# Performance work log

Hardware: AMD Instinct MI355X
Metric: run time of the kernel (lower is better)

## Reference

```python
import jax, jax.numpy as jnp
import numpy as np

B, CIN, T = 32, 16, 4096
H, DEPTH, E, K = 192, 4, 4, 7
DILATIONS = (1, 2, 4, 8)
NUM_BANDS, P = 16, 8
HM = 2 * H  # mlp_ratio = 2.0
NCLS = 50
GAIN_LIMIT = 0.5
EPS = 1e-5


def _rbf_basis(num_bins, num_bands):
    freqs = jnp.linspace(0.0, 1.0, num_bins)
    centers = jnp.linspace(0.0, 1.0, num_bands)
    width = 1.5 / (num_bands - 1)
    basis = jnp.exp(-0.5 * ((freqs[None, :] - centers[:, None]) / width) ** 2)
    return basis / jnp.clip(basis.sum(-1, keepdims=True), 1e-8)


def _layernorm(x, g, b):
    m = x.mean(-1, keepdims=True)
    v = x.var(-1, keepdims=True)
    return (x - m) / jnp.sqrt(v + EPS) * g + b


def _groupnorm1(x, g, b):
    # GroupNorm(1, C): normalize over (C, T) per sample, per-channel affine
    m = x.mean((1, 2), keepdims=True)
    v = x.var((1, 2), keepdims=True)
    return (x - m) / jnp.sqrt(v + EPS) * g[None, :, None] + b[None, :, None]


def _bn_eval(x, g, b):
    # eval-mode BatchNorm1d with running_mean=0, running_var=1
    return x * (g / jnp.sqrt(1.0 + EPS))[None, :, None] + b[None, :, None]


def _gelu(x):
    return jax.nn.gelu(x, approximate=False)


def _dwconv(x, w, dilation):
    pad = (K // 2) * dilation
    return jax.lax.conv_general_dilated(
        x, w, (1,), [(pad, pad)], rhs_dilation=(dilation,),
        dimension_numbers=("NCH", "OIH", "NCH"), feature_group_count=x.shape[1])


def setup_inputs() -> dict:
    key = jax.random.key(0)
    ks = jax.random.split(key, 12)
    return {
        "x": jax.random.normal(ks[0], (B, CIN, T), jnp.float32),
        "stem_w": jax.random.normal(ks[1], (H, CIN, 3)) * 0.1,
        "stem_bn_g": jnp.ones((H,)), "stem_bn_b": jnp.zeros((H,)),
        "ln_g": jnp.ones((NUM_BANDS,)), "ln_b": jnp.zeros((NUM_BANDS,)),
        "proj_w": jax.random.normal(ks[2], (NUM_BANDS, NUM_BANDS)) * 0.25,
        "prototypes": jax.random.normal(ks[3], (P, NUM_BANDS)) * 0.02,
        "route_lib": jax.random.normal(ks[4], (P, DEPTH, E)) * 0.1,
        "gain_lib": jax.random.normal(ks[5], (P, DEPTH, H)) * 0.1,
        "norm1_g": jnp.ones((DEPTH, H)), "norm1_b": jnp.zeros((DEPTH, H)),
        "expert_w": jax.random.normal(ks[6], (DEPTH, E, H, 1, K)) * 0.2,
        "mix_w": jax.random.normal(ks[7], (DEPTH, H, H)) * (1.0 / np.sqrt(H)),
        "mix_bn_g": jnp.ones((DEPTH, H)), "mix_bn_b": jnp.zeros((DEPTH, H)),
        "norm2_g": jnp.ones((DEPTH, H)), "norm2_b": jnp.zeros((DEPTH, H)),
        "mlp_w1": jax.random.normal(ks[8], (DEPTH, HM, H)) * (1.0 / np.sqrt(H)),
        "mlp_b1": jnp.zeros((DEPTH, HM)),
        "mlp_w2": jax.random.normal(ks[9], (DEPTH, H, HM)) * (1.0 / np.sqrt(HM)),
        "mlp_b2": jnp.zeros((DEPTH, H)),
        "head_w": jax.random.normal(ks[10], (NCLS, H)) * (1.0 / np.sqrt(H)),
        "head_b": jnp.zeros((NCLS,)),
    }


def reference(x, stem_w, stem_bn_g, stem_bn_b, ln_g, ln_b, proj_w, prototypes,
              route_lib, gain_lib, norm1_g, norm1_b, expert_w, mix_w, mix_bn_g,
              mix_bn_b, norm2_g, norm2_b, mlp_w1, mlp_b1, mlp_w2, mlp_b2,
              head_w, head_b):
    # --- SpectralSummary ---
    spec = jnp.fft.rfft(x.astype(jnp.float32), axis=-1, norm="ortho")
    mag = jnp.abs(spec).mean(axis=1)                      # [B, bins]
    basis = _rbf_basis(mag.shape[-1], NUM_BANDS)          # [bands, bins]
    summary = jnp.log1p(mag) @ basis.T                    # [B, bands]
    # --- PrototypeRouter ---
    s = _layernorm(summary, ln_g, ln_b)
    rs = s @ proj_w.T
    logits = -((rs[:, None, :] - prototypes[None]) ** 2).mean(-1)  # [B, P]
    assign = jax.nn.softmax(logits * np.sqrt(NUM_BANDS), axis=-1)
    routes = jax.nn.softmax(jnp.einsum("bp,pde->bde", assign, route_lib), axis=-1)  # [B,D,E]
    gains = 1.0 + GAIN_LIMIT * jnp.tanh(jnp.einsum("bp,pdc->bdc", assign, gain_lib))  # [B,D,C]
    # --- Backbone stem ---
    z = jax.lax.conv_general_dilated(x, stem_w, (1,), [(1, 1)],
                                     dimension_numbers=("NCH", "OIH", "NCH"))
    z = _gelu(_bn_eval(z, stem_bn_g, stem_bn_b))
    # --- Routed temporal blocks ---
    for d in range(DEPTH):
        zn = _groupnorm1(z, norm1_g[d], norm1_b[d])
        pieces = jnp.stack([_dwconv(zn, expert_w[d, e], DILATIONS[e]) for e in range(E)], axis=1)  # [B,E,C,T]
        mixed = jnp.einsum("be,bect->bct", routes[:, d], pieces)
        mixed = mixed * gains[:, d][:, :, None]
        mixed = _gelu(_bn_eval(jnp.einsum("oc,bct->bot", mix_w[d], mixed), mix_bn_g[d], mix_bn_b[d]))
        z = z + mixed
        zn2 = _groupnorm1(z, norm2_g[d], norm2_b[d])
        h = _gelu(jnp.einsum("oc,bct->bot", mlp_w1[d], zn2) + mlp_b1[d][None, :, None])
        z = z + jnp.einsum("oc,bct->bot", mlp_w2[d], h) + mlp_b2[d][None, :, None]
    # --- Head: global average pool + linear ---
    pooled = z.mean(-1)
    return pooled @ head_w.T + head_b
```

## Files before the change

### kernel.cpp

```cpp
#include <hip/hip_runtime.h>
#include <math.h>

constexpr int cB = 32, cCIN = 16, cT = 4096, cH = 192, cD = 4, cE = 4, cK = 7;
constexpr int cBANDS = 16, cP = 8, cHM = 384, cNCLS = 50, cBINS = 2049;
constexpr float cEPS = 1e-5f;
constexpr int TT = 64, HALO = 24;
constexpr int ZSTR = 112;
constexpr int NTAP = 19;
constexpr float INV_SQRT2 = 0.7071067811865475f;

typedef __bf16 bf16_t;
typedef bf16_t bf16x8 __attribute__((ext_vector_type(8)));
typedef float f32x4 __attribute__((ext_vector_type(4)));

constexpr int OFFS[NTAP] = {-24,-16,-12,-8,-6,-4,-3,-2,-1,0,1,2,3,4,6,8,12,16,24};
constexpr int IDXT[cE][cK] = {
    {6, 7, 8, 9, 10, 11, 12},
    {4, 5, 7, 9, 11, 13, 14},
    {2, 3, 5, 9, 13, 15, 16},
    {0, 1, 3, 9, 15, 17, 18}};

__device__ __forceinline__ int xcd_swz(int bid) {
    return (bid & 7) * 256 + (bid >> 3);
}

__device__ __forceinline__ float fast_erf(float x) {
    float ax = fabsf(x);
    float t = 1.0f / fmaf(0.3275911f, ax, 1.0f);
    float p = t * fmaf(t, fmaf(t, fmaf(t, fmaf(t, 1.061405429f, -1.453152027f),
                                       1.421413741f), -0.284496736f), 0.254829592f);
    float e = __expf(-ax * ax);
    float r = 1.0f - p * e;
    return copysignf(r, x);
}
__device__ __forceinline__ float gelu_exact(float v) {
    return 0.5f * v * (1.0f + fast_erf(v * INV_SQRT2));
}
__device__ __forceinline__ unsigned short f2bf(float f) {
    union { float f; unsigned u; } v; v.f = f;
    unsigned r = (v.u + 0x7FFFu + ((v.u >> 16) & 1u)) >> 16;
    return (unsigned short)r;
}
__device__ __forceinline__ float bf2f(unsigned short u) {
    union { unsigned u; float f; } v; v.u = ((unsigned)u) << 16;
    return v.f;
}

__global__ __launch_bounds__(256) void k_zero(float* __restrict__ p, int n) {
    int i = blockIdx.x * 256 + threadIdx.x;
    if (i < n) p[i] = 0.f;
}

__global__ __launch_bounds__(256) void k_cvt(const float* __restrict__ src,
                                             unsigned short* __restrict__ dst, int n) {
    int i = blockIdx.x * 256 + threadIdx.x;
    if (i < n) dst[i] = f2bf(src[i]);
}

__global__ __launch_bounds__(256) void k_twiddle(float2* __restrict__ tw) {
    int ls = blockIdx.x;
    int n = cT >> ls;
    int cnt = n >> 1;
    int base = cT - (cT >> ls);
    for (int p = threadIdx.x; p < cnt; p += 256) {
        float ang = -6.283185307179586f * (float)p / (float)n;
        float sv, cv;
        sincosf(ang, &sv, &cv);
        tw[base + p] = make_float2(cv, sv);
    }
}

__global__ __launch_bounds__(256) void k_fft_mag(const float* __restrict__ x,
                                                 const float2* __restrict__ tw,
                                                 float* __restrict__ mag) {
    constexpr int N2 = cT / 2;
    __shared__ float Sr[2][N2];
    __shared__ float Si[2][N2];
    int b = blockIdx.x / cCIN, c = blockIdx.x % cCIN;
    const float* xp = x + ((size_t)b * cCIN + c) * cT;
    for (int t = threadIdx.x; t < N2; t += 256) {
        float2 v = *reinterpret_cast<const float2*>(&xp[2 * t]);
        Sr[0][t] = v.x; Si[0][t] = v.y;
    }
    __syncthreads();
    int cur = 0;
    for (int ls = 0; ls < 11; ls++) {
        int s = 1 << ls;
        int twb = cT - (cT >> (ls + 1));
        for (int j = threadIdx.x; j < N2 / 2; j += 256) {
            int p = j >> ls;
            float2 w = tw[twb + p];
            float wr = w.x, wi = w.y;
            int ia = j, ib = j + N2 / 2;
            float ar = Sr[cur][ia], ai = Si[cur][ia];
            float br = Sr[cur][ib], bi = Si[cur][ib];
            int oa = j + (j & ~(s - 1));
            int ob = oa + s;
            Sr[cur ^ 1][oa] = ar + br;
            Si[cur ^ 1][oa] = ai + bi;
            float tr = ar - br, ti = ai - bi;
            Sr[cur ^ 1][ob] = tr * wr - ti * wi;
            Si[cur ^ 1][ob] = tr * wi + ti * wr;
        }
        __syncthreads();
        cur ^= 1;
    }
    const float scale = (1.0f / 64.0f) * (1.0f / 16.0f);
    for (int k = threadIdx.x; k <= N2; k += 256) {
        int k2 = k & (N2 - 1), km = (N2 - k) & (N2 - 1);
        float yr = Sr[cur][k2], yi = Si[cur][k2];
        float zr = Sr[cur][km], zi = Si[cur][km];
        float Ar = 0.5f * (yr + zr), Ai = 0.5f * (yi - zi);
        float Br = 0.5f * (yi + zi), Bi = -0.5f * (yr - zr);
        float wr, wi;
        if (k < N2) { float2 w = tw[k]; wr = w.x; wi = w.y; }
        else { wr = -1.f; wi = 0.f; }
        float Xr = Ar + wr * Br - wi * Bi;
        float Xi = Ai + wr * Bi + wi * Br;
        atomicAdd(&mag[b * cBINS + k], sqrtf(Xr * Xr + Xi * Xi) * scale);
    }
}

__global__ __launch_bounds__(256) void k_basis(float* __restrict__ basis) {
    __shared__ float vals[cBINS];
    __shared__ float red[256];
    int band = blockIdx.x;
    float cb = (float)band / 15.0f;
    float inv_w = 15.0f / 1.5f;
    float local = 0.f;
    for (int k = threadIdx.x; k < cBINS; k += 256) {
        float f = (float)k / 2048.0f;
        float u = (f - cb) * inv_w;
        float v = expf(-0.5f * u * u);
        vals[k] = v;
        local += v;
    }
    red[threadIdx.x] = local;
    __syncthreads();
    for (int s = 128; s > 0; s >>= 1) {
        if (threadIdx.x < s) red[threadIdx.x] += red[threadIdx.x + s];
        __syncthreads();
    }
    float inv_sum = 1.0f / fmaxf(red[0], 1e-8f);
    for (int k = threadIdx.x; k < cBINS; k += 256)
        basis[band * cBINS + k] = vals[k] * inv_sum;
}

__global__ __launch_bounds__(256) void k_summary(const float* __restrict__ mag,
                                                 const float* __restrict__ basis,
                                                 float* __restrict__ summary) {
    int b = blockIdx.x;
    float acc[cBANDS];
#pragma unroll
    for (int i = 0; i < cBANDS; i++) acc[i] = 0.f;
    for (int k = threadIdx.x; k < cBINS; k += 256) {
        float lm = log1pf(mag[b * cBINS + k]);
#pragma unroll
        for (int band = 0; band < cBANDS; band++) acc[band] += lm * basis[band * cBINS + k];
    }
    __shared__ float red[cBANDS][256];
#pragma unroll
    for (int band = 0; band < cBANDS; band++) red[band][threadIdx.x] = acc[band];
    __syncthreads();
    for (int s = 128; s > 0; s >>= 1) {
        if (threadIdx.x < s)
#pragma unroll
            for (int band = 0; band < cBANDS; band++)
                red[band][threadIdx.x] += red[band][threadIdx.x + s];
        __syncthreads();
    }
    if (threadIdx.x < cBANDS) summary[b * cBANDS + threadIdx.x] = red[threadIdx.x][0];
}

__global__ __launch_bounds__(64) void k_router(
    const float* __restrict__ summary, const float* __restrict__ ln_g,
    const float* __restrict__ ln_b, const float* __restrict__ proj_w,
    const float* __restrict__ prototypes, const float* __restrict__ route_lib,
    const float* __restrict__ gain_lib, float* __restrict__ routes,
    float* __restrict__ gains) {
    int b = threadIdx.x;
    if (b >= cB) return;
    float s[cBANDS];
    float mean = 0.f;
#pragma unroll
    for (int i = 0; i < cBANDS; i++) { s[i] = summary[b * cBANDS + i]; mean += s[i]; }
    mean *= (1.0f / cBANDS);
    float var = 0.f;
#pragma unroll
    for (int i = 0; i < cBANDS; i++) { float d = s[i] - mean; var += d * d; }
    var *= (1.0f / cBANDS);
    float rstd = rsqrtf(var + cEPS);
#pragma unroll
    for (int i = 0; i < cBANDS; i++) s[i] = (s[i] - mean) * rstd * ln_g[i] + ln_b[i];
    float rs[cBANDS];
#pragma unroll
    for (int j = 0; j < cBANDS; j++) {
        float a = 0.f;
#pragma unroll
        for (int i = 0; i < cBANDS; i++) a += s[i] * proj_w[j * cBANDS + i];
        rs[j] = a;
    }
    float logits[cP];
    float mx = -1e30f;
#pragma unroll
    for (int p = 0; p < cP; p++) {
        float a = 0.f;
#pragma unroll
        for (int j = 0; j < cBANDS; j++) {
            float d = rs[j] - prototypes[p * cBANDS + j];
            a += d * d;
        }
        logits[p] = -(a * (1.0f / cBANDS)) * 4.0f;
        mx = fmaxf(mx, logits[p]);
    }
    float assign[cP];
    float denom = 0.f;
#pragma unroll
    for (int p = 0; p < cP; p++) { assign[p] = expf(logits[p] - mx); denom += assign[p]; }
    float invden = 1.0f / denom;
#pragma unroll
    for (int p = 0; p < cP; p++) assign[p] *= invden;
    for (int d = 0; d < cD; d++) {
        float r[cE];
        float rmx = -1e30f;
#pragma unroll
        for (int e = 0; e < cE; e++) {
            float a = 0.f;
#pragma unroll
            for (int p = 0; p < cP; p++) a += assign[p] * route_lib[(p * cD + d) * cE + e];
            r[e] = a;
            rmx = fmaxf(rmx, a);
        }
        float rden = 0.f;
#pragma unroll
        for (int e = 0; e < cE; e++) { r[e] = expf(r[e] - rmx); rden += r[e]; }
        float rinv = 1.0f / rden;
#pragma unroll
        for (int e = 0; e < cE; e++) routes[(b * cD + d) * cE + e] = r[e] * rinv;
        for (int c = 0; c < cH; c++) {
            float a = 0.f;
#pragma unroll
            for (int p = 0; p < cP; p++) a += assign[p] * gain_lib[(p * cD + d) * cH + c];
            gains[((size_t)b * cD + d) * cH + c] = 1.0f + 0.5f * tanhf(a);
        }
    }
}

__global__ __launch_bounds__(192) void k_weff(const float* __restrict__ ew_all,
                                              const float* __restrict__ routes,
                                              unsigned short* __restrict__ weff_g) {
    int bd = blockIdx.x;
    int d = bd % cD;
    int c = threadIdx.x;
    float rte[cE];
#pragma unroll
    for (int e = 0; e < cE; e++) rte[e] = routes[bd * cE + e];
    float acc[NTAP];
#pragma unroll
    for (int o = 0; o < NTAP; o++) acc[o] = 0.f;
#pragma unroll
    for (int e = 0; e < cE; e++) {
#pragma unroll
        for (int k = 0; k < cK; k++)
            acc[IDXT[e][k]] += rte[e] * ew_all[(((size_t)d * cE + e) * cH + c) * cK + k];
    }
    unsigned short* dst = weff_g + ((size_t)bd * cH + c) * 20;
#pragma unroll
    for (int o = 0; o < NTAP; o++) dst[o] = f2bf(acc[o]);
    dst[NTAP] = 0;
}

constexpr int STT = 256;
__global__ __launch_bounds__(256) void k_stem(const float* __restrict__ x,
                                              const float* __restrict__ stem_w,
                                              const float* __restrict__ bn_g,
                                              const float* __restrict__ bn_b,
                                              float* __restrict__ z,
                                              float* __restrict__ sums_out) {
    __shared__ float xs[cCIN][STT + 2];
    __shared__ float ws[cH * cCIN * 3];
    int blk = blockIdx.x;
    int b = blk / (cT / STT);
    int t0 = (blk % (cT / STT)) * STT;
    for (int i = threadIdx.x; i < cH * cCIN * 3; i += 256) ws[i] = stem_w[i];
    for (int i = threadIdx.x; i < cCIN * (STT + 2); i += 256) {
        int c = i / (STT + 2), tt = i % (STT + 2);
        int gt = t0 + tt - 1;
        xs[c][tt] = (gt >= 0 && gt < cT) ? x[((size_t)b * cCIN + c) * cT + gt] : 0.f;
    }
    __syncthreads();
    int tt = threadIdx.x;
    float xv[cCIN][3];
#pragma unroll
    for (int c = 0; c < cCIN; c++)
#pragma unroll
        for (int k = 0; k < 3; k++) xv[c][k] = xs[c][tt + k];
    int gt = t0 + tt;
    float bnrs = rsqrtf(1.0f + cEPS);
    float s = 0.f, q = 0.f;
    for (int h = 0; h < cH; h++) {
        const float* w = &ws[h * cCIN * 3];
        float acc = 0.f;
#pragma unroll
        for (int c = 0; c < cCIN; c++)
#pragma unroll
            for (int k = 0; k < 3; k++) acc += xv[c][k] * w[c * 3 + k];
        float v = acc * (bn_g[h] * bnrs) + bn_b[h];
        float res = gelu_exact(v);
        z[((size_t)b * cH + h) * cT + gt] = res;
        s += res; q += res * res;
    }
#pragma unroll
    for (int off = 32; off > 0; off >>= 1) { s += __shfl_down(s, off); q += __shfl_down(q, off); }
    if ((threadIdx.x & 63) == 0) {
        atomicAdd(&sums_out[b * 2], s);
        atomicAdd(&sums_out[b * 2 + 1], q);
    }
}

__global__ __launch_bounds__(256, 2) void k_block1(
    const float* __restrict__ zin, float* __restrict__ zout,
    const float* __restrict__ sums_in, float* __restrict__ sums_out,
    const float* __restrict__ g1, const float* __restrict__ b1,
    const unsigned short* __restrict__ weff_g, const unsigned short* __restrict__ mwb,
    const float* __restrict__ mg, const float* __restrict__ mb,
    const float* __restrict__ gains, int d) {
    __shared__ unsigned short zn[cH][ZSTR];
    __shared__ unsigned short mxT[TT][200];
    int blk = xcd_swz(blockIdx.x);
    int b = blk / (cT / TT);
    int t0 = (blk % (cT / TT)) * TT;
    int tid = threadIdx.x;
    const float invN = 1.0f / (float)(cH * cT);
    float mean = sums_in[b * 2] * invN;
    float var = sums_in[b * 2 + 1] * invN - mean * mean;
    float rstd = rsqrtf(var + cEPS);
    for (int u = tid; u < cH * 28; u += 256) {
        int c = u / 28, tt = (u % 28) * 4;
        int gt = t0 + tt - HALO;
        float gc = g1[c], bc = b1[c];
        float n0, n1, n2, n3;
        if (gt >= 0 && gt + 3 < cT) {
            float4 v = *reinterpret_cast<const float4*>(&zin[((size_t)b * cH + c) * cT + gt]);
            n0 = (v.x - mean) * rstd * gc + bc;
            n1 = (v.y - mean) * rstd * gc + bc;
            n2 = (v.z - mean) * rstd * gc + bc;
            n3 = (v.w - mean) * rstd * gc + bc;
        } else {
            const float* zp = &zin[((size_t)b * cH + c) * cT];
            n0 = (gt + 0 >= 0 && gt + 0 < cT) ? (zp[gt + 0] - mean) * rstd * gc + bc : 0.f;
            n1 = (gt + 1 >= 0 && gt + 1 < cT) ? (zp[gt + 1] - mean) * rstd * gc + bc : 0.f;
            n2 = (gt + 2 >= 0 && gt + 2 < cT) ? (zp[gt + 2] - mean) * rstd * gc + bc : 0.f;
            n3 = (gt + 3 >= 0 && gt + 3 < cT) ? (zp[gt + 3] - mean) * rstd * gc + bc : 0.f;
        }
        ushort4 pk;
        pk.x = f2bf(n0); pk.y = f2bf(n1); pk.z = f2bf(n2); pk.w = f2bf(n3);
        *reinterpret_cast<ushort4*>(&zn[c][tt]) = pk;
    }
    int lane = tid & 63, wid = tid >> 6;
    int lrow = lane & 15;
    int lk8 = (lane >> 4) << 3;
    int r0 = (lane >> 4) << 2;
    int mbase = wid * 48;
    float res[3][4][4];
#pragma unroll
    for (int mt = 0; mt < 3; mt++)
#pragma unroll
        for (int nt = 0; nt < 4; nt++)
#pragma unroll
            for (int r = 0; r < 4; r++)
                res[mt][nt][r] = zin[((size_t)b * cH + mbase + mt * 16 + r0 + r) * cT +
                                     t0 + nt * 16 + lrow];
    __syncthreads();
    if (tid < cH) {
        int c = tid;
        const unsigned short* wp = weff_g + ((size_t)(b * cD + d) * cH + c) * 20;
        float wv[NTAP];
#pragma unroll
        for (int o = 0; o < NTAP; o++) wv[o] = bf2f(wp[o]);
        float g = gains[((size_t)b * cD + d) * cH + c];
        float win[ZSTR];
#pragma unroll
        for (int v = 0; v < 14; v++) {
            bf16x8 w8 = *reinterpret_cast<const bf16x8*>(&zn[c][8 * v]);
#pragma unroll
            for (int u = 0; u < 8; u++) win[8 * v + u] = (float)w8[u];
        }
#pragma unroll
        for (int t = 0; t < TT; t++) {
            float a = 0.f;
#pragma unroll
            for (int o = 0; o < NTAP; o++)
                a = fmaf(wv[o], win[t + HALO + OFFS[o]], a);
            mxT[t][c] = f2bf(a * g);
        }
    }
    __syncthreads();
    f32x4 acc[3][4];
#pragma unroll
    for (int mt = 0; mt < 3; mt++)
#pragma unroll
        for (int nt = 0; nt < 4; nt++)
#pragma unroll
            for (int r = 0; r < 4; r++) acc[mt][nt][r] = 0.f;
    for (int kk = 0; kk < 6; kk++) {
        int k0 = kk * 32 + lk8;
        bf16x8 a0 = *reinterpret_cast<const bf16x8*>(&mwb[(size_t)(mbase + lrow) * cH + k0]);
        bf16x8 a1 = *reinterpret_cast<const bf16x8*>(&mwb[(size_t)(mbase + 16 + lrow) * cH + k0]);
        bf16x8 a2 = *reinterpret_cast<const bf16x8*>(&mwb[(size_t)(mbase + 32 + lrow) * cH + k0]);
#pragma unroll
        for (int nt = 0; nt < 4; nt++) {
            bf16x8 bf = *reinterpret_cast<const bf16x8*>(&mxT[nt * 16 + lrow][k0]);
            acc[0][nt] = __builtin_amdgcn_mfma_f32_16x16x32_bf16(a0, bf, acc[0][nt], 0, 0, 0);
            acc[1][nt] = __builtin_amdgcn_mfma_f32_16x16x32_bf16(a1, bf, acc[1][nt], 0, 0, 0);
            acc[2][nt] = __builtin_amdgcn_mfma_f32_16x16x32_bf16(a2, bf, acc[2][nt], 0, 0, 0);
        }
    }
    float bnrs = rsqrtf(1.0f + cEPS);
    float s = 0.f, q = 0.f;
#pragma unroll
    for (int mt = 0; mt < 3; mt++) {
#pragma unroll
        for (int nt = 0; nt < 4; nt++) {
#pragma unroll
            for (int r = 0; r < 4; r++) {
                int o = mbase + mt * 16 + r0 + r;
                int t = t0 + nt * 16 + lrow;
                size_t idx = ((size_t)b * cH + o) * cT + t;
                float val = res[mt][nt][r] + gelu_exact(acc[mt][nt][r] * (mg[o] * bnrs) + mb[o]);
                zout[idx] = val;
                s += val; q += val * val;
            }
        }
    }
#pragma unroll
    for (int off = 32; off > 0; off >>= 1) { s += __shfl_down(s, off); q += __shfl_down(q, off); }
    if (lane == 0) {
        atomicAdd(&sums_out[b * 2], s);
        atomicAdd(&sums_out[b * 2 + 1], q);
    }
}

__global__ __launch_bounds__(256, 2) void k_block2(
    float* __restrict__ z, const float* __restrict__ sums_in,
    float* __restrict__ sums_out,
    const float* __restrict__ g2, const float* __restrict__ b2,
    const unsigned short* __restrict__ w1b, const float* __restrict__ bb1,
    const unsigned short* __restrict__ w2b, const float* __restrict__ bb2) {
    __shared__ unsigned short znT[TT][200];
    __shared__ unsigned short hT[TT][392];
    int blk = xcd_swz(blockIdx.x);
    int b = blk / (cT / TT);
    int t0 = (blk % (cT / TT)) * TT;
    const float invN = 1.0f / (float)(cH * cT);
    float mean = sums_in[b * 2] * invN;
    float var = sums_in[b * 2 + 1] * invN - mean * mean;
    float rstd = rsqrtf(var + cEPS);
    for (int i = threadIdx.x; i < cH * (TT / 4); i += 256) {
        int c = i >> 4, t4 = (i & 15) << 2;
        float4 v = *reinterpret_cast<const float4*>(&z[((size_t)b * cH + c) * cT + t0 + t4]);
        float gc = g2[c], bc = b2[c];
        znT[t4 + 0][c] = f2bf((v.x - mean) * rstd * gc + bc);
        znT[t4 + 1][c] = f2bf((v.y - mean) * rstd * gc + bc);
        znT[t4 + 2][c] = f2bf((v.z - mean) * rstd * gc + bc);
        znT[t4 + 3][c] = f2bf((v.w - mean) * rstd * gc + bc);
    }
    int lane = threadIdx.x & 63, wid = threadIdx.x >> 6;
    int lrow = lane & 15;
    int lk8 = (lane >> 4) << 3;
    int r0 = (lane >> 4) << 2;
    float res[3][4][4];
    {
        int mb2 = wid * 48;
#pragma unroll
        for (int mt = 0; mt < 3; mt++)
#pragma unroll
            for (int nt = 0; nt < 4; nt++)
#pragma unroll
                for (int r = 0; r < 4; r++)
                    res[mt][nt][r] = z[((size_t)b * cH + mb2 + mt * 16 + r0 + r) * cT +
                                       t0 + nt * 16 + lrow];
    }
    __syncthreads();
    for (int chunk = 0; chunk < 2; chunk++) {
        int mbase = wid * 96 + chunk * 48;
        f32x4 acc[3][4];
#pragma unroll
        for (int mt = 0; mt < 3; mt++) {
#pragma unroll
            for (int r = 0; r < 4; r++) {
                float bv = bb1[mbase + mt * 16 + r0 + r];
                acc[mt][0][r] = bv; acc[mt][1][r] = bv; acc[mt][2][r] = bv; acc[mt][3][r] = bv;
            }
        }
        for (int kk = 0; kk < 6; kk++) {
            int k0 = kk * 32 + lk8;
            bf16x8 a0 = *reinterpret_cast<const bf16x8*>(&w1b[(size_t)(mbase + lrow) * cH + k0]);
            bf16x8 a1 = *reinterpret_cast<const bf16x8*>(&w1b[(size_t)(mbase + 16 + lrow) * cH + k0]);
            bf16x8 a2 = *reinterpret_cast<const bf16x8*>(&w1b[(size_t)(mbase + 32 + lrow) * cH + k0]);
#pragma unroll
            for (int nt = 0; nt < 4; nt++) {
                bf16x8 bf = *reinterpret_cast<const bf16x8*>(&znT[nt * 16 + lrow][k0]);
                acc[0][nt] = __builtin_amdgcn_mfma_f32_16x16x32_bf16(a0, bf, acc[0][nt], 0, 0, 0);
                acc[1][nt] = __builtin_amdgcn_mfma_f32_16x16x32_bf16(a1, bf, acc[1][nt], 0, 0, 0);
                acc[2][nt] = __builtin_amdgcn_mfma_f32_16x16x32_bf16(a2, bf, acc[2][nt], 0, 0, 0);
            }
        }
#pragma unroll
        for (int mt = 0; mt < 3; mt++) {
            int o0 = mbase + mt * 16 + r0;
#pragma unroll
            for (int nt = 0; nt < 4; nt++) {
                int t = nt * 16 + lrow;
                ushort4 pk;
                pk.x = f2bf(gelu_exact(acc[mt][nt][0]));
                pk.y = f2bf(gelu_exact(acc[mt][nt][1]));
                pk.z = f2bf(gelu_exact(acc[mt][nt][2]));
                pk.w = f2bf(gelu_exact(acc[mt][nt][3]));
                *reinterpret_cast<ushort4*>(&hT[t][o0]) = pk;
            }
        }
    }
    __syncthreads();
    {
        int mbase = wid * 48;
        f32x4 acc[3][4];
#pragma unroll
        for (int mt = 0; mt < 3; mt++) {
#pragma unroll
            for (int r = 0; r < 4; r++) {
                float bv = bb2[mbase + mt * 16 + r0 + r];
                acc[mt][0][r] = bv; acc[mt][1][r] = bv; acc[mt][2][r] = bv; acc[mt][3][r] = bv;
            }
        }
        for (int kk = 0; kk < 12; kk++) {
            int k0 = kk * 32 + lk8;
            bf16x8 a0 = *reinterpret_cast<const bf16x8*>(&w2b[(size_t)(mbase + lrow) * cHM + k0]);
            bf16x8 a1 = *reinterpret_cast<const bf16x8*>(&w2b[(size_t)(mbase + 16 + lrow) * cHM + k0]);
            bf16x8 a2 = *reinterpret_cast<const bf16x8*>(&w2b[(size_t)(mbase + 32 + lrow) * cHM + k0]);
#pragma unroll
            for (int nt = 0; nt < 4; nt++) {
                bf16x8 bf = *reinterpret_cast<const bf16x8*>(&hT[nt * 16 + lrow][k0]);
                acc[0][nt] = __builtin_amdgcn_mfma_f32_16x16x32_bf16(a0, bf, acc[0][nt], 0, 0, 0);
                acc[1][nt] = __builtin_amdgcn_mfma_f32_16x16x32_bf16(a1, bf, acc[1][nt], 0, 0, 0);
                acc[2][nt] = __builtin_amdgcn_mfma_f32_16x16x32_bf16(a2, bf, acc[2][nt], 0, 0, 0);
            }
        }
        float s = 0.f, q = 0.f;
#pragma unroll
        for (int mt = 0; mt < 3; mt++) {
#pragma unroll
            for (int nt = 0; nt < 4; nt++) {
#pragma unroll
                for (int r = 0; r < 4; r++) {
                    int o = mbase + mt * 16 + r0 + r;
                    int t = t0 + nt * 16 + lrow;
                    size_t idx = ((size_t)b * cH + o) * cT + t;
                    float val = res[mt][nt][r] + acc[mt][nt][r];
                    z[idx] = val;
                    s += val; q += val * val;
                }
            }
        }
#pragma unroll
        for (int off = 32; off > 0; off >>= 1) { s += __shfl_down(s, off); q += __shfl_down(q, off); }
        if (lane == 0) {
            atomicAdd(&sums_out[b * 2], s);
            atomicAdd(&sums_out[b * 2 + 1], q);
        }
    }
}

__global__ __launch_bounds__(256) void k_pool(const float* __restrict__ z,
                                              float* __restrict__ pooled) {
    int bh = blockIdx.x;
    const float* zp = z + (size_t)bh * cT;
    float s = 0.f;
    for (int t = threadIdx.x; t < cT; t += 256) s += zp[t];
    __shared__ float red[256];
    red[threadIdx.x] = s;
    __syncthreads();
    for (int st = 128; st > 0; st >>= 1) {
        if (threadIdx.x < st) red[threadIdx.x] += red[threadIdx.x + st];
        __syncthreads();
    }
    if (threadIdx.x == 0) pooled[bh] = red[0] * (1.0f / cT);
}

__global__ __launch_bounds__(256) void k_head(const float* __restrict__ pooled,
                                              const float* __restrict__ hw,
                                              const float* __restrict__ hb,
                                              float* __restrict__ out) {
    int i = blockIdx.x * 256 + threadIdx.x;
    if (i >= cB * cNCLS) return;
    int b = i / cNCLS, n = i % cNCLS;
    float acc = hb[n];
    const float* pw = pooled + b * cH;
    const float* wr = hw + n * cH;
    for (int h = 0; h < cH; h++) acc += pw[h] * wr[h];
    out[i] = acc;
}

extern "C" void kernel_launch(void* const* d_in, const int* in_sizes, int n_in,
                              void* d_out, int out_size, void* d_ws, size_t ws_size,
                              hipStream_t stream) {
    const float* x          = (const float*)d_in[0];
    const float* stem_w     = (const float*)d_in[1];
    const float* stem_bn_g  = (const float*)d_in[2];
    const float* stem_bn_b  = (const float*)d_in[3];
    const float* ln_g       = (const float*)d_in[4];
    const float* ln_b       = (const float*)d_in[5];
    const float* proj_w     = (const float*)d_in[6];
    const float* prototypes = (const float*)d_in[7];
    const float* route_lib  = (const float*)d_in[8];
    const float* gain_lib   = (const float*)d_in[9];
    const float* norm1_g    = (const float*)d_in[10];
    const float* norm1_b    = (const float*)d_in[11];
    const float* expert_w   = (const float*)d_in[12];
    const float* mix_w      = (const float*)d_in[13];
    const float* mix_bn_g   = (const float*)d_in[14];
    const float* mix_bn_b   = (const float*)d_in[15];
    const float* norm2_g    = (const float*)d_in[16];
    const float* norm2_b    = (const float*)d_in[17];
    const float* mlp_w1     = (const float*)d_in[18];
    const float* mlp_b1     = (const float*)d_in[19];
    const float* mlp_w2     = (const float*)d_in[20];
    const float* mlp_b2     = (const float*)d_in[21];
    const float* head_w     = (const float*)d_in[22];
    const float* head_b     = (const float*)d_in[23];

    float* ws = (float*)d_ws;
    size_t off = 0;
    const size_t ZN = (size_t)cB * cH * cT;
    float* zA      = ws + off; off += ZN;
    float* zB      = ws + off; off += ZN;
    float* mag     = ws + off; off += (size_t)cB * cBINS;
    float* sums    = ws + off; off += 9 * cB * 2;
    float* basis   = ws + off; off += (size_t)cBANDS * cBINS;
    float* summary = ws + off; off += cB * cBANDS;
    float* routes  = ws + off; off += cB * cD * cE;
    float* gains   = ws + off; off += (size_t)cB * cD * cH;
    float* pooled  = ws + off; off += cB * cH;
    float2* tw     = (float2*)(ws + off); off += 2 * (cT - 1) + 2;
    unsigned short* mixb = (unsigned short*)(ws + off); off += (size_t)cD * cH * cH / 2;
    unsigned short* w1b  = (unsigned short*)(ws + off); off += (size_t)cD * cHM * cH / 2;
    unsigned short* w2b  = (unsigned short*)(ws + off); off += (size_t)cD * cH * cHM / 2;
    unsigned short* weff = (unsigned short*)(ws + off); off += (size_t)cB * cD * cH * 20 / 2;

    int nz = cB * cBINS + 9 * cB * 2;
    k_zero<<<(nz + 255) / 256, 256, 0, stream>>>(mag, nz);

    k_cvt<<<(cD * cH * cH + 255) / 256, 256, 0, stream>>>(mix_w, mixb, cD * cH * cH);
    k_cvt<<<(cD * cHM * cH + 255) / 256, 256, 0, stream>>>(mlp_w1, w1b, cD * cHM * cH);
    k_cvt<<<(cD * cH * cHM + 255) / 256, 256, 0, stream>>>(mlp_w2, w2b, cD * cH * cHM);

    k_twiddle<<<12, 256, 0, stream>>>(tw);
    k_fft_mag<<<cB * cCIN, 256, 0, stream>>>(x, tw, mag);
    k_basis<<<cBANDS, 256, 0, stream>>>(basis);
    k_summary<<<cB, 256, 0, stream>>>(mag, basis, summary);
    k_router<<<1, 64, 0, stream>>>(summary, ln_g, ln_b, proj_w, prototypes,
                                   route_lib, gain_lib, routes, gains);
    k_weff<<<cB * cD, 192, 0, stream>>>(expert_w, routes, weff);

    k_stem<<<cB * (cT / STT), 256, 0, stream>>>(x, stem_w, stem_bn_g, stem_bn_b, zA,
                                                sums + 0 * cB * 2);

    float* zi = zA;
    float* zo = zB;
    for (int d = 0; d < cD; d++) {
        k_block1<<<cB * (cT / TT), 256, 0, stream>>>(
            zi, zo, sums + (size_t)(2 * d) * cB * 2, sums + (size_t)(2 * d + 1) * cB * 2,
            norm1_g + d * cH, norm1_b + d * cH,
            weff, mixb + (size_t)d * cH * cH,
            mix_bn_g + d * cH, mix_bn_b + d * cH, gains, d);
        k_block2<<<cB * (cT / TT), 256, 0, stream>>>(
            zo, sums + (size_t)(2 * d + 1) * cB * 2, sums + (size_t)(2 * d + 2) * cB * 2,
            norm2_g + d * cH, norm2_b + d * cH,
            w1b + (size_t)d * cHM * cH, mlp_b1 + d * cHM,
            w2b + (size_t)d * cH * cHM, mlp_b2 + d * cH);
        float* t = zi; zi = zo; zo = t;
    }

    k_pool<<<cB * cH, 256, 0, stream>>>(zi, pooled);
    k_head<<<(cB * cNCLS + 255) / 256, 256, 0, stream>>>(pooled, head_w, head_b,
                                                         (float*)d_out);
}
```

Measured before the change: 1.275 ms.

## Split MLP hidden into two chunks interleaved with second GEMM to cut LDS

```diff
diff --git a/kernel.cpp b/kernel.cpp
--- a/kernel.cpp
+++ b/kernel.cpp
@@ -55,6 +55,21 @@
                                              unsigned short* __restrict__ dst, int n) {
     int i = blockIdx.x * 256 + threadIdx.x;
     if (i < n) dst[i] = f2bf(src[i]);
+}
+
+__global__ __launch_bounds__(256) void k_cvt_w2perm(const float* __restrict__ src,
+                                                    unsigned short* __restrict__ dst, int n) {
+    int j = blockIdx.x * 256 + threadIdx.x;
+    if (j >= n) return;
+    int dd = j / (cH * cHM);
+    int rem = j % (cH * cHM);
+    int o = rem / cHM, m = rem % cHM;
+    int wid = m / 96;
+    int rr = m % 96;
+    int chunk = rr / 48;
+    int ii = rr % 48;
+    int pos = chunk * 192 + wid * 48 + ii;
+    dst[(size_t)dd * cH * cHM + (size_t)o * cHM + pos] = f2bf(src[j]);
 }
 
 __global__ __launch_bounds__(256) void k_twiddle(float2* __restrict__ tw) {
@@ -441,14 +456,14 @@
     }
 }
 
-__global__ __launch_bounds__(256, 2) void k_block2(
+__global__ __launch_bounds__(256, 3) void k_block2(
     float* __restrict__ z, const float* __restrict__ sums_in,
     float* __restrict__ sums_out,
     const float* __restrict__ g2, const float* __restrict__ b2,
     const unsigned short* __restrict__ w1b, const float* __restrict__ bb1,
-    const unsigned short* __restrict__ w2b, const float* __restrict__ bb2) {
+    const unsigned short* __restrict__ w2p, const float* __restrict__ bb2) {
     __shared__ unsigned short znT[TT][200];
-    __shared__ unsigned short hT[TT][392];
+    __shared__ unsigned short hT[TT][200];
     int blk = xcd_swz(blockIdx.x);
     int b = blk / (cT / TT);
     int t0 = (blk % (cT / TT)) * TT;
@@ -465,32 +480,30 @@
         znT[t4 + 2][c] = f2bf((v.z - mean) * rstd * gc + bc);
         znT[t4 + 3][c] = f2bf((v.w - mean) * rstd * gc + bc);
     }
+    __syncthreads();
     int lane = threadIdx.x & 63, wid = threadIdx.x >> 6;
     int lrow = lane & 15;
     int lk8 = (lane >> 4) << 3;
     int r0 = (lane >> 4) << 2;
-    float res[3][4][4];
-    {
-        int mb2 = wid * 48;
-#pragma unroll
-        for (int mt = 0; mt < 3; mt++)
-#pragma unroll
-            for (int nt = 0; nt < 4; nt++)
-#pragma unroll
-                for (int r = 0; r < 4; r++)
-                    res[mt][nt][r] = z[((size_t)b * cH + mb2 + mt * 16 + r0 + r) * cT +
-                                       t0 + nt * 16 + lrow];
-    }
-    __syncthreads();
+    int obase = wid * 48;
+    f32x4 acc2[3][4];
+#pragma unroll
+    for (int mt = 0; mt < 3; mt++) {
+#pragma unroll
+        for (int r = 0; r < 4; r++) {
+            float bv = bb2[obase + mt * 16 + r0 + r];
+            acc2[mt][0][r] = bv; acc2[mt][1][r] = bv; acc2[mt][2][r] = bv; acc2[mt][3][r] = bv;
+        }
+    }
     for (int chunk = 0; chunk < 2; chunk++) {
         int mbase = wid * 96 + chunk * 48;
-        f32x4 acc[3][4];
+        f32x4 acc1[3][4];
 #pragma unroll
         for (int mt = 0; mt < 3; mt++) {
 #pragma unroll
             for (int r = 0; r < 4; r++) {
                 float bv = bb1[mbase + mt * 16 + r0 + r];
-                acc[mt][0][r] = bv; acc[mt][1][r] = bv; acc[mt][2][r] = bv; acc[mt][3][r] = bv;
+                acc1[mt][0][r] = bv; acc1[mt][1][r] = bv; acc1[mt][2][r] = bv; acc1[mt][3][r] = bv;
             }
         }
         for (int kk = 0; kk < 6; kk++) {
@@ -501,73 +514,63 @@
 #pragma unroll
             for (int nt = 0; nt < 4; nt++) {
                 bf16x8 bf = *reinterpret_cast<const bf16x8*>(&znT[nt * 16 + lrow][k0]);
-                acc[0][nt] = __builtin_amdgcn_mfma_f32_16x16x32_bf16(a0, bf, acc[0][nt], 0, 0, 0);
-                acc[1][nt] = __builtin_amdgcn_mfma_f32_16x16x32_bf16(a1, bf, acc[1][nt], 0, 0, 0);
-                acc[2][nt] = __builtin_amdgcn_mfma_f32_16x16x32_bf16(a2, bf, acc[2][nt], 0, 0, 0);
+                acc1[0][nt] = __builtin_amdgcn_mfma_f32_16x16x32_bf16(a0, bf, acc1[0][nt], 0, 0, 0);
+                acc1[1][nt] = __builtin_amdgcn_mfma_f32_16x16x32_bf16(a1, bf, acc1[1][nt], 0, 0, 0);
+                acc1[2][nt] = __builtin_amdgcn_mfma_f32_16x16x32_bf16(a2, bf, acc1[2][nt], 0, 0, 0);
             }
         }
 #pragma unroll
         for (int mt = 0; mt < 3; mt++) {
-            int o0 = mbase + mt * 16 + r0;
+            int o0 = wid * 48 + mt * 16 + r0;
 #pragma unroll
             for (int nt = 0; nt < 4; nt++) {
                 int t = nt * 16 + lrow;
                 ushort4 pk;
-                pk.x = f2bf(gelu_exact(acc[mt][nt][0]));
-                pk.y = f2bf(gelu_exact(acc[mt][nt][1]));
-                pk.z = f2bf(gelu_exact(acc[mt][nt][2]));
-                pk.w = f2bf(gelu_exact(acc[mt][nt][3]));
+                pk.x = f2bf(gelu_exact(acc1[mt][nt][0]));
+                pk.y = f2bf(gelu_exact(acc1[mt][nt][1]));
+                pk.z = f2bf(gelu_exact(acc1[mt][nt][2]));
+                pk.w = f2bf(gelu_exact(acc1[mt][nt][3]));
                 *reinterpret_cast<ushort4*>(&hT[t][o0]) = pk;
             }
         }
-    }
-    __syncthreads();
-    {
-        int mbase = wid * 48;
-        f32x4 acc[3][4];
-#pragma unroll
-        for (int mt = 0; mt < 3; mt++) {
+        __syncthreads();
+        for (int kk = 0; kk < 6; kk++) {
+            int kl = kk * 32 + lk8;
+            int kg = chunk * 192 + kl;
+            bf16x8 a0 = *reinterpret_cast<const bf16x8*>(&w2p[(size_t)(obase + lrow) * cHM + kg]);
+            bf16x8 a1 = *reinterpret_cast<const bf16x8*>(&w2p[(size_t)(obase + 16 + lrow) * cHM + kg]);
+            bf16x8 a2 = *reinterpret_cast<const bf16x8*>(&w2p[(size_t)(obase + 32 + lrow) * cHM + kg]);
+#pragma unroll
+            for (int nt = 0; nt < 4; nt++) {
+                bf16x8 bf = *reinterpret_cast<const bf16x8*>(&hT[nt * 16 + lrow][kl]);
+                acc2[0][nt] = __builtin_amdgcn_mfma_f32_16x16x32_bf16(a0, bf, acc2[0][nt], 0, 0, 0);
+                acc2[1][nt] = __builtin_amdgcn_mfma_f32_16x16x32_bf16(a1, bf, acc2[1][nt], 0, 0, 0);
+                acc2[2][nt] = __builtin_amdgcn_mfma_f32_16x16x32_bf16(a2, bf, acc2[2][nt], 0, 0, 0);
+            }
+        }
+        if (chunk == 0) __syncthreads();
+    }
+    float s = 0.f, q = 0.f;
+#pragma unroll
+    for (int mt = 0; mt < 3; mt++) {
+#pragma unroll
+        for (int nt = 0; nt < 4; nt++) {
 #pragma unroll
             for (int r = 0; r < 4; r++) {
-                float bv = bb2[mbase + mt * 16 + r0 + r];
-                acc[mt][0][r] = bv; acc[mt][1][r] = bv; acc[mt][2][r] = bv; acc[mt][3][r] = bv;
+                int o = obase + mt * 16 + r0 + r;
+                int t = t0 + nt * 16 + lrow;
+                size_t idx = ((size_t)b * cH + o) * cT + t;
+                float val = z[idx] + acc2[mt][nt][r];
+                z[idx] = val;
+                s += val; q += val * val;
             }
         }
-        for (int kk = 0; kk < 12; kk++) {
-            int k0 = kk * 32 + lk8;
-            bf16x8 a0 = *reinterpret_cast<const bf16x8*>(&w2b[(size_t)(mbase + lrow) * cHM + k0]);
-            bf16x8 a1 = *reinterpret_cast<const bf16x8*>(&w2b[(size_t)(mbase + 16 + lrow) * cHM + k0]);
-            bf16x8 a2 = *reinterpret_cast<const bf16x8*>(&w2b[(size_t)(mbase + 32 + lrow) * cHM + k0]);
-#pragma unroll
-            for (int nt = 0; nt < 4; nt++) {
-                bf16x8 bf = *reinterpret_cast<const bf16x8*>(&hT[nt * 16 + lrow][k0]);
-                acc[0][nt] = __builtin_amdgcn_mfma_f32_16x16x32_bf16(a0, bf, acc[0][nt], 0, 0, 0);
-                acc[1][nt] = __builtin_amdgcn_mfma_f32_16x16x32_bf16(a1, bf, acc[1][nt], 0, 0, 0);
-                acc[2][nt] = __builtin_amdgcn_mfma_f32_16x16x32_bf16(a2, bf, acc[2][nt], 0, 0, 0);
-            }
-        }
-        float s = 0.f, q = 0.f;
-#pragma unroll
-        for (int mt = 0; mt < 3; mt++) {
-#pragma unroll
-            for (int nt = 0; nt < 4; nt++) {
-#pragma unroll
-                for (int r = 0; r < 4; r++) {
-                    int o = mbase + mt * 16 + r0 + r;
-                    int t = t0 + nt * 16 + lrow;
-                    size_t idx = ((size_t)b * cH + o) * cT + t;
-                    float val = res[mt][nt][r] + acc[mt][nt][r];
-                    z[idx] = val;
-                    s += val; q += val * val;
-                }
-            }
-        }
-#pragma unroll
-        for (int off = 32; off > 0; off >>= 1) { s += __shfl_down(s, off); q += __shfl_down(q, off); }
-        if (lane == 0) {
-            atomicAdd(&sums_out[b * 2], s);
-            atomicAdd(&sums_out[b * 2 + 1], q);
-        }
+    }
+#pragma unroll
+    for (int off = 32; off > 0; off >>= 1) { s += __shfl_down(s, off); q += __shfl_down(q, off); }
+    if (lane == 0) {
+        atomicAdd(&sums_out[b * 2], s);
+        atomicAdd(&sums_out[b * 2 + 1], q);
     }
 }
 
@@ -652,7 +655,7 @@
 
     k_cvt<<<(cD * cH * cH + 255) / 256, 256, 0, stream>>>(mix_w, mixb, cD * cH * cH);
     k_cvt<<<(cD * cHM * cH + 255) / 256, 256, 0, stream>>>(mlp_w1, w1b, cD * cHM * cH);
-    k_cvt<<<(cD * cH * cHM + 255) / 256, 256, 0, stream>>>(mlp_w2, w2b, cD * cH * cHM);
+    k_cvt_w2perm<<<(cD * cH * cHM + 255) / 256, 256, 0, stream>>>(mlp_w2, w2b, cD * cH * cHM);
 
     k_twiddle<<<12, 256, 0, stream>>>(tw);
     k_fft_mag<<<cB * cCIN, 256, 0, stream>>>(x, tw, mag);
```

Result: no change. 1.298 ms (+1.7%).
